# Kernel optimization log

Hardware: AMD Instinct MI355X
Metric: run time of the kernel (lower is better)

The kernel has to match this reference:

```python
import jax, jax.numpy as jnp
import numpy as np

N = 100000
E = 600000
NODE_DIM = 128
EDGE_DIM = 32
HIDDEN = 128  # must equal NODE_DIM (index_add_ into zeros_like(node_features))


def _linear_params(key, fan_in, fan_out):
    kw, kb = jax.random.split(key)
    bound = 1.0 / np.sqrt(fan_in)
    W = jax.random.uniform(kw, (fan_in, fan_out), minval=-bound, maxval=bound, dtype=jnp.float32)
    b = jax.random.uniform(kb, (fan_out,), minval=-bound, maxval=bound, dtype=jnp.float32)
    return W, b


def setup_inputs() -> dict:
    key = jax.random.key(0)
    ks = jax.random.split(key, 8)
    node_features = jax.random.normal(ks[0], (N, NODE_DIM), dtype=jnp.float32)
    edge_index = jax.random.randint(ks[1], (2, E), 0, N, dtype=jnp.int32)
    edge_features = jax.random.normal(ks[2], (E, EDGE_DIM), dtype=jnp.float32)
    m_W1, m_b1 = _linear_params(ks[3], 2 * NODE_DIM + EDGE_DIM, HIDDEN)
    m_W2, m_b2 = _linear_params(ks[4], HIDDEN, HIDDEN)
    a_W, a_b = _linear_params(ks[5], HIDDEN, 1)
    u_W1, u_b1 = _linear_params(ks[6], NODE_DIM + HIDDEN, HIDDEN)
    u_W2, u_b2 = _linear_params(ks[7], HIDDEN, NODE_DIM)
    return {
        "node_features": node_features,
        "edge_features": edge_features,
        "m_W1": m_W1, "m_b1": m_b1, "m_W2": m_W2, "m_b2": m_b2,
        "a_W": a_W, "a_b": a_b,
        "u_W1": u_W1, "u_b1": u_b1, "u_W2": u_W2, "u_b2": u_b2,
        "edge_index": edge_index,
    }


def reference(node_features, edge_features, m_W1, m_b1, m_W2, m_b2,
              a_W, a_b, u_W1, u_b1, u_W2, u_b2, edge_index):
    row, col = edge_index[0], edge_index[1]
    # gather endpoints + edge feats -> [E, 2*node_dim + edge_dim]
    msg_in = jnp.concatenate([node_features[row], node_features[col], edge_features], axis=-1)
    # message MLP
    h = jax.nn.relu(msg_in @ m_W1 + m_b1)
    messages = h @ m_W2 + m_b2  # [E, hidden]
    # global softmax over all edges (dim=0), per attention column (width 1)
    attn = jax.nn.softmax(messages @ a_W + a_b, axis=0)  # [E, 1]
    messages = messages * attn
    # scatter-add into destination nodes
    aggregated = jax.ops.segment_sum(messages, col, num_segments=node_features.shape[0])
    # update MLP + residual
    upd_in = jnp.concatenate([node_features, aggregated], axis=-1)
    u = jax.nn.relu(upd_in @ u_W1 + u_b1)
    updated = u @ u_W2 + u_b2
    return updated + node_features
```

## Files before the change

### kernel.cpp

```cpp
#include <hip/hip_runtime.h>
#include <hip/hip_bf16.h>
#include <hip/hip_fp8.h>
#include <stdint.h>

#define NN 100000
#define NE 600000
#define ND 128
#define ED 32
#define HID 128
#define SCANB 391
#define NEB 4688

using short8 = __attribute__((ext_vector_type(8))) short;
using f32x4  = __attribute__((ext_vector_type(4))) float;
using f32x2  = __attribute__((ext_vector_type(2))) float;

__device__ __forceinline__ uint32_t f2bf(float f) {
  uint32_t u = __float_as_uint(f);
  return (u + 0x7FFFu + ((u >> 16) & 1u)) >> 16;
}
__device__ __forceinline__ float bf2f(uint32_t h) {
  return __uint_as_float(h << 16);
}
__device__ __forceinline__ short8 pack8(float4 a, float4 b) {
  short8 s;
  s[0] = (short)f2bf(a.x); s[1] = (short)f2bf(a.y);
  s[2] = (short)f2bf(a.z); s[3] = (short)f2bf(a.w);
  s[4] = (short)f2bf(b.x); s[5] = (short)f2bf(b.y);
  s[6] = (short)f2bf(b.z); s[7] = (short)f2bf(b.w);
  return s;
}

__device__ __forceinline__ uint8_t fp8_enc(float v) {
#if __has_builtin(__builtin_amdgcn_cvt_pk_fp8_f32)
  return (uint8_t)(__builtin_amdgcn_cvt_pk_fp8_f32(v, v, 0, false) & 0xFF);
#else
  __hip_fp8_e4m3 q(v);
  return q.__x;
#endif
}
__device__ __forceinline__ float2 fp8_dec2(uint32_t v) {
#if __has_builtin(__builtin_amdgcn_cvt_pk_f32_fp8)
  f32x2 r = __builtin_amdgcn_cvt_pk_f32_fp8((int)v, false);
  return make_float2(r[0], r[1]);
#else
  __hip_fp8_e4m3 qa, qb;
  qa.__x = (uint8_t)(v & 0xFF); qb.__x = (uint8_t)((v >> 8) & 0xFF);
  return make_float2((float)qa, (float)qb);
#endif
}

__global__ __launch_bounds__(256) void k_prep_all(
    const float* __restrict__ uW1, const float* __restrict__ uW2,
    const float* __restrict__ W1, const float* __restrict__ W2,
    short* __restrict__ U1p, short* __restrict__ U2p,
    uint8_t* __restrict__ W1p8, uint8_t* __restrict__ W2p8) {
  int o = blockIdx.x * 256 + threadIdx.x;
  const float* src; int rel; int isFp8;
  short* dstS = nullptr; uint8_t* dst8 = nullptr;
  if (o < 32768)       { rel = o;         src = uW1; dstS = U1p;  isFp8 = 0; }
  else if (o < 49152)  { rel = o - 32768; src = uW2; dstS = U2p;  isFp8 = 0; }
  else if (o < 86016)  { rel = o - 49152; src = W1;  dst8 = W1p8; isFp8 = 1; }
  else if (o < 102400) { rel = o - 86016; src = W2;  dst8 = W2p8; isFp8 = 1; }
  else return;
  int j = rel & 7, c16 = (rel >> 3) & 15, g = (rel >> 7) & 3, nt = (rel >> 9) & 7, c = rel >> 12;
  int k = c * 32 + g * 8 + j, n = nt * 16 + c16;
  float v = src[k * 128 + n];
  if (isFp8) dst8[rel] = fp8_enc(v);
  else       dstS[rel] = (short)f2bf(v);
}

__global__ __launch_bounds__(256) void k_prep_nf(const float* __restrict__ nf,
                                                 short* __restrict__ nfb,
                                                 uint8_t* __restrict__ nfb8,
                                                 int* __restrict__ cnt) {
  const int total = NN * ND / 8;
  int gid = blockIdx.x * 256 + threadIdx.x;
  for (int i = gid; i < NN; i += gridDim.x * 256) cnt[i] = 0;
  for (int u = gid; u < total; u += gridDim.x * 256) {
    const float* s = nf + (size_t)u * 8;
    float4 v0 = *(const float4*)s, v1 = *(const float4*)(s + 4);
    *(short8*)(nfb + (size_t)u * 8) = pack8(v0, v1);
    uint8_t b[8];
    b[0] = fp8_enc(v0.x); b[1] = fp8_enc(v0.y); b[2] = fp8_enc(v0.z); b[3] = fp8_enc(v0.w);
    b[4] = fp8_enc(v1.x); b[5] = fp8_enc(v1.y); b[6] = fp8_enc(v1.z); b[7] = fp8_enc(v1.w);
    *(uint2*)(nfb8 + (size_t)u * 8) = *(const uint2*)b;
  }
}

__global__ __launch_bounds__(256, 3) void k_edge_mfma(
    const uint8_t* __restrict__ nfb8, const float* __restrict__ ef,
    const uint8_t* __restrict__ W1p8, const float* __restrict__ b1,
    const uint8_t* __restrict__ W2p8, const float* __restrict__ b2,
    const float* __restrict__ aW, const int* __restrict__ ei,
    const int* __restrict__ perm,
    uint8_t* __restrict__ msg8, float* __restrict__ logits) {
  __shared__ __align__(16) uint8_t sRow[128 * 136];
  __shared__ __align__(16) uint8_t sCol[128 * 136];
  __shared__ __align__(16) uint8_t sEf[128 * 40];
  __shared__ __align__(16) uint8_t sB8[2][4096];
  __shared__ int sIdx[256];
  __shared__ int sPerm[128];

  const int tid = threadIdx.x;
  const int wv = tid >> 6, ln = tid & 63, cr = ln & 15, gp = ln >> 4;
  const int e0 = blockIdx.x * 128;
  const int wrow = wv * 32;

  if (tid < 128) {
    int e = e0 + tid; if (e >= NE) e = NE - 1;
    sIdx[tid] = ei[e];
    sIdx[128 + tid] = ei[NE + e];
    sPerm[tid] = perm[e];
  }
  __syncthreads();

#pragma unroll
  for (int it = 0; it < 16; ++it) {
    int t = it * 256 + tid;
    int side = t >> 11;
    int r = (t & 2047) >> 4;
    int o = (t & 15) * 8;
    const uint8_t* src = nfb8 + (size_t)sIdx[side * 128 + r] * ND + o;
    uint8_t* dst = (side ? sCol : sRow) + r * 136 + o;
    *(uint2*)dst = *(const uint2*)src;
  }
#pragma unroll
  for (int it = 0; it < 2; ++it) {
    int u = it * 256 + tid;
    int r = u >> 2, o = (u & 3) * 8;
    int e = e0 + r; if (e >= NE) e = NE - 1;
    const float* src = ef + (size_t)e * ED + o;
    float4 v0 = *(const float4*)src, v1 = *(const float4*)(src + 4);
    uint8_t b[8];
    b[0] = fp8_enc(v0.x); b[1] = fp8_enc(v0.y); b[2] = fp8_enc(v0.z); b[3] = fp8_enc(v0.w);
    b[4] = fp8_enc(v1.x); b[5] = fp8_enc(v1.y); b[6] = fp8_enc(v1.z); b[7] = fp8_enc(v1.w);
    *(uint2*)&sEf[r * 40 + o] = *(const uint2*)b;
  }
  *(uint4*)&sB8[0][tid * 16] = *(const uint4*)(W1p8 + tid * 16);

  float bia[8], aWr[8], bia2[8];
#pragma unroll
  for (int nt = 0; nt < 8; ++nt) {
    bia[nt] = b1[nt * 16 + cr];
    bia2[nt] = b2[nt * 16 + cr];
    aWr[nt] = aW[nt * 16 + cr];
  }
  f32x4 acc[2][8];
#pragma unroll
  for (int mt = 0; mt < 2; ++mt)
#pragma unroll
    for (int nt = 0; nt < 8; ++nt)
      acc[mt][nt] = (f32x4){bia[nt], bia[nt], bia[nt], bia[nt]};
  __syncthreads();

  for (int c = 0; c < 9; ++c) {
    if (c < 8)
      *(uint4*)&sB8[(c + 1) & 1][tid * 16] =
          *(const uint4*)(W1p8 + (c + 1) * 4096 + tid * 16);
    const uint8_t* aSrc = (c < 4) ? (sRow + c * 32)
                        : (c < 8) ? (sCol + (c - 4) * 32) : sEf;
    const int pitch = (c == 8) ? 40 : 136;
    long af0 = *(const long*)(aSrc + (wrow + cr) * pitch + gp * 8);
    long af1 = *(const long*)(aSrc + (wrow + 16 + cr) * pitch + gp * 8);
    const uint8_t* bbuf = sB8[c & 1];
#pragma unroll
    for (int nt = 0; nt < 8; ++nt) {
      long bfr = *(const long*)&bbuf[(nt * 4 + gp) * 128 + cr * 8];
      acc[0][nt] = __builtin_amdgcn_mfma_f32_16x16x32_fp8_fp8(af0, bfr, acc[0][nt], 0, 0, 0);
      acc[1][nt] = __builtin_amdgcn_mfma_f32_16x16x32_fp8_fp8(af1, bfr, acc[1][nt], 0, 0, 0);
    }
    __syncthreads();
  }

#pragma unroll
  for (int mt = 0; mt < 2; ++mt)
#pragma unroll
    for (int nt = 0; nt < 8; ++nt)
#pragma unroll
      for (int rr = 0; rr < 4; ++rr)
        sRow[(wrow + mt * 16 + gp * 4 + rr) * 136 + nt * 16 + cr] =
            fp8_enc(fmaxf(acc[mt][nt][rr], 0.f));
  *(uint4*)&sB8[0][tid * 16] = *(const uint4*)(W2p8 + tid * 16);
  __syncthreads();

  f32x4 acc2[2][8];
#pragma unroll
  for (int mt = 0; mt < 2; ++mt)
#pragma unroll
    for (int nt = 0; nt < 8; ++nt)
      acc2[mt][nt] = (f32x4){bia2[nt], bia2[nt], bia2[nt], bia2[nt]};
  for (int c2 = 0; c2 < 4; ++c2) {
    if (c2 < 3)
      *(uint4*)&sB8[(c2 + 1) & 1][tid * 16] =
          *(const uint4*)(W2p8 + (c2 + 1) * 4096 + tid * 16);
    long af0 = *(const long*)&sRow[(wrow + cr) * 136 + c2 * 32 + gp * 8];
    long af1 = *(const long*)&sRow[(wrow + 16 + cr) * 136 + c2 * 32 + gp * 8];
    const uint8_t* bbuf = sB8[c2 & 1];
#pragma unroll
    for (int nt = 0; nt < 8; ++nt) {
      long bfr = *(const long*)&bbuf[(nt * 4 + gp) * 128 + cr * 8];
      acc2[0][nt] = __builtin_amdgcn_mfma_f32_16x16x32_fp8_fp8(af0, bfr, acc2[0][nt], 0, 0, 0);
      acc2[1][nt] = __builtin_amdgcn_mfma_f32_16x16x32_fp8_fp8(af1, bfr, acc2[1][nt], 0, 0, 0);
    }
    __syncthreads();
  }

#pragma unroll
  for (int mt = 0; mt < 2; ++mt)
#pragma unroll
    for (int rr = 0; rr < 4; ++rr) {
      float p = 0.f;
#pragma unroll
      for (int nt = 0; nt < 8; ++nt) p += acc2[mt][nt][rr] * aWr[nt];
      p += __shfl_xor(p, 1, 64);
      p += __shfl_xor(p, 2, 64);
      p += __shfl_xor(p, 4, 64);
      p += __shfl_xor(p, 8, 64);
      int row = wrow + mt * 16 + gp * 4 + rr;
      if (cr == 0 && e0 + row < NE) logits[sPerm[row]] = p;
    }

#pragma unroll
  for (int mt = 0; mt < 2; ++mt)
#pragma unroll
    for (int nt = 0; nt < 8; ++nt)
#pragma unroll
      for (int rr = 0; rr < 4; ++rr)
        sCol[(wrow + mt * 16 + gp * 4 + rr) * 136 + nt * 16 + cr] =
            fp8_enc(acc2[mt][nt][rr]);
  __syncthreads();
#pragma unroll
  for (int it = 0; it < 8; ++it) {
    int row = it * 16 + (tid >> 4), o8 = (tid & 15) * 8;
    if (e0 + row < NE)
      *(uint2*)(msg8 + (size_t)sPerm[row] * HID + o8) = *(const uint2*)&sCol[row * 136 + o8];
  }
}

__global__ __launch_bounds__(256, 4) void k_node_mfma(
    const short* __restrict__ nfb, const short* __restrict__ aggb,
    const short* __restrict__ U1p, const float* __restrict__ b1,
    const short* __restrict__ U2p, const float* __restrict__ b2,
    float* __restrict__ out) {
  __shared__ __align__(16) short sH[128 * 136];

  const int tid = threadIdx.x;
  const int wv = tid >> 6, ln = tid & 63, cr = ln & 15, gp = ln >> 4;
  const int n0 = blockIdx.x * 128;
  const int wrow = wv * 32;

  int na0 = n0 + wrow + cr;      if (na0 >= NN) na0 = NN - 1;
  int na1 = n0 + wrow + 16 + cr; if (na1 >= NN) na1 = NN - 1;

  float bia[8], bia2[8];
#pragma unroll
  for (int nt = 0; nt < 8; ++nt) {
    bia[nt] = b1[nt * 16 + cr];
    bia2[nt] = b2[nt * 16 + cr];
  }
  f32x4 acc[2][8];
#pragma unroll
  for (int mt = 0; mt < 2; ++mt)
#pragma unroll
    for (int nt = 0; nt < 8; ++nt)
      acc[mt][nt] = (f32x4){bia[nt], bia[nt], bia[nt], bia[nt]};

#pragma unroll
  for (int c = 0; c < 8; ++c) {
    const short* base = (c < 4) ? nfb : aggb;
    const int ko = (c & 3) * 32 + gp * 8;
    short8 af0 = *(const short8*)(base + (size_t)na0 * ND + ko);
    short8 af1 = *(const short8*)(base + (size_t)na1 * ND + ko);
    const short* Wc = U1p + c * 4096;
#pragma unroll
    for (int nt = 0; nt < 8; ++nt) {
      short8 bfr = *(const short8*)(Wc + (nt * 4 + gp) * 128 + cr * 8);
      acc[0][nt] = __builtin_amdgcn_mfma_f32_16x16x32_bf16(af0, bfr, acc[0][nt], 0, 0, 0);
      acc[1][nt] = __builtin_amdgcn_mfma_f32_16x16x32_bf16(af1, bfr, acc[1][nt], 0, 0, 0);
    }
  }

#pragma unroll
  for (int mt = 0; mt < 2; ++mt)
#pragma unroll
    for (int nt = 0; nt < 8; ++nt)
#pragma unroll
      for (int rr = 0; rr < 4; ++rr)
        sH[(wrow + mt * 16 + gp * 4 + rr) * 136 + nt * 16 + cr] =
            (short)f2bf(fmaxf(acc[mt][nt][rr], 0.f));

  f32x4 acc2[2][8];
#pragma unroll
  for (int mt = 0; mt < 2; ++mt)
#pragma unroll
    for (int nt = 0; nt < 8; ++nt)
      acc2[mt][nt] = (f32x4){bia2[nt], bia2[nt], bia2[nt], bia2[nt]};
#pragma unroll
  for (int c2 = 0; c2 < 4; ++c2) {
    short8 af0 = *(const short8*)&sH[(wrow + cr) * 136 + c2 * 32 + gp * 8];
    short8 af1 = *(const short8*)&sH[(wrow + 16 + cr) * 136 + c2 * 32 + gp * 8];
    const short* Wc = U2p + c2 * 4096;
#pragma unroll
    for (int nt = 0; nt < 8; ++nt) {
      short8 bfr = *(const short8*)(Wc + (nt * 4 + gp) * 128 + cr * 8);
      acc2[0][nt] = __builtin_amdgcn_mfma_f32_16x16x32_bf16(af0, bfr, acc2[0][nt], 0, 0, 0);
      acc2[1][nt] = __builtin_amdgcn_mfma_f32_16x16x32_bf16(af1, bfr, acc2[1][nt], 0, 0, 0);
    }
  }

#pragma unroll
  for (int mt = 0; mt < 2; ++mt)
#pragma unroll
    for (int rr = 0; rr < 4; ++rr) {
      int n = n0 + wrow + mt * 16 + gp * 4 + rr;
      if (n < NN) {
#pragma unroll
        for (int nt = 0; nt < 8; ++nt) {
          int col = nt * 16 + cr;
          float r = bf2f((uint16_t)nfb[(size_t)n * ND + col]);
          out[(size_t)n * ND + col] = acc2[mt][nt][rr] + r;
        }
      }
    }
}

__device__ __forceinline__ void ms_combine(float& m, float& s, float m2, float s2) {
  float M = fmaxf(m, m2);
  s = s * expf(m - M) + s2 * expf(m2 - M);
  m = M;
}
__device__ __forceinline__ void ms_block_reduce(float& m, float& s) {
#pragma unroll
  for (int o = 1; o < 64; o <<= 1) {
    float m2 = __shfl_xor(m, o, 64), s2 = __shfl_xor(s, o, 64);
    ms_combine(m, s, m2, s2);
  }
  __shared__ float sm[4], ss[4];
  if ((threadIdx.x & 63) == 0) { sm[threadIdx.x >> 6] = m; ss[threadIdx.x >> 6] = s; }
  __syncthreads();
  m = sm[0]; s = ss[0];
  ms_combine(m, s, sm[1], ss[1]);
  ms_combine(m, s, sm[2], ss[2]);
  ms_combine(m, s, sm[3], ss[3]);
}
__global__ __launch_bounds__(256) void k_red_p(const float* __restrict__ logits,
                                               float* __restrict__ pmax,
                                               float* __restrict__ psum) {
  float m = -3.402823466e38f, s = 0.f;
  for (int i = blockIdx.x * 256 + threadIdx.x; i < NE; i += 1024 * 256) {
    float l = logits[i];
    if (l <= m) s += expf(l - m);
    else { s = s * expf(m - l) + 1.f; m = l; }
  }
  ms_block_reduce(m, s);
  if (threadIdx.x == 0) { pmax[blockIdx.x] = m; psum[blockIdx.x] = s; }
}
__global__ __launch_bounds__(256) void k_red_f(const float* __restrict__ pmax,
                                               const float* __restrict__ psum,
                                               float* __restrict__ red) {
  float m = pmax[threadIdx.x], s = psum[threadIdx.x];
  ms_combine(m, s, pmax[threadIdx.x + 256], psum[threadIdx.x + 256]);
  ms_combine(m, s, pmax[threadIdx.x + 512], psum[threadIdx.x + 512]);
  ms_combine(m, s, pmax[threadIdx.x + 768], psum[threadIdx.x + 768]);
  ms_block_reduce(m, s);
  if (threadIdx.x == 0) { red[0] = m; red[1] = 1.0f / s; }
}

__global__ __launch_bounds__(256) void k_hist(const int* __restrict__ ei,
                                              int* __restrict__ cnt) {
  int e = blockIdx.x * 256 + threadIdx.x;
  if (e < NE) atomicAdd(&cnt[ei[NE + e]], 1);
}
__global__ __launch_bounds__(256) void k_scan_bsum(const int* __restrict__ cnt,
                                                   int* __restrict__ bsum) {
  int i = blockIdx.x * 256 + threadIdx.x;
  int v = (i < NN) ? cnt[i] : 0;
#pragma unroll
  for (int s = 1; s < 64; s <<= 1) v += __shfl_xor(v, s, 64);
  __shared__ int sv[4];
  if ((threadIdx.x & 63) == 0) sv[threadIdx.x >> 6] = v;
  __syncthreads();
  if (threadIdx.x == 0) bsum[blockIdx.x] = sv[0] + sv[1] + sv[2] + sv[3];
}
__global__ __launch_bounds__(512) void k_scan_boff(const int* __restrict__ bsum,
                                                   int* __restrict__ boff,
                                                   int* __restrict__ rowptr) {
  __shared__ int s[512];
  int t = threadIdx.x;
  int v = (t < SCANB) ? bsum[t] : 0;
  s[t] = v;
  __syncthreads();
  for (int off = 1; off < 512; off <<= 1) {
    int u = (t >= off) ? s[t - off] : 0;
    __syncthreads();
    s[t] += u;
    __syncthreads();
  }
  if (t < SCANB) boff[t] = s[t] - v;
  if (t == 0) rowptr[NN] = NE;
}
__global__ __launch_bounds__(256) void k_scan_final(int* __restrict__ cnt,
                                                    const int* __restrict__ boff,
                                                    int* __restrict__ rowptr) {
  __shared__ int s[256];
  int b = blockIdx.x, t = threadIdx.x, i = b * 256 + t;
  int v = (i < NN) ? cnt[i] : 0;
  s[t] = v;
  __syncthreads();
  for (int off = 1; off < 256; off <<= 1) {
    int u = (t >= off) ? s[t - off] : 0;
    __syncthreads();
    s[t] += u;
    __syncthreads();
  }
  int excl = s[t] - v + boff[b];
  if (i < NN) { rowptr[i] = excl; cnt[i] = excl; }
}
__global__ __launch_bounds__(256) void k_fill(const int* __restrict__ ei,
                                              int* __restrict__ cursor,
                                              int* __restrict__ perm) {
  int e = blockIdx.x * 256 + threadIdx.x;
  if (e >= NE) return;
  int c = ei[NE + e];
  int pos = atomicAdd(&cursor[c], 1);
  perm[e] = pos;
}

__global__ __launch_bounds__(256) void k_agg(
    const uint8_t* __restrict__ msg8, const float* __restrict__ logits,
    const int* __restrict__ rowptr, const float* __restrict__ red,
    short* __restrict__ aggb) {
  int n = blockIdx.x * 4 + (threadIdx.x >> 6);
  int lane = threadIdx.x & 63;
  if (n >= NN) return;
  float gm = red[0], inv = red[1];
  int i0 = rowptr[n], i1 = rowptr[n + 1];
  float a0 = 0.f, a1 = 0.f;
  for (int i = i0; i < i1; ++i) {
    float wt = expf(logits[i] - gm) * inv;
    uint32_t pk = *(const uint16_t*)(msg8 + (size_t)i * HID + lane * 2);
    float2 d = fp8_dec2(pk);
    a0 += wt * d.x;
    a1 += wt * d.y;
  }
  uint32_t packed = f2bf(a0) | (f2bf(a1) << 16);
  *(uint32_t*)(aggb + (size_t)n * ND + lane * 2) = packed;
}

extern "C" void kernel_launch(void* const* d_in, const int* in_sizes, int n_in,
                              void* d_out, int out_size, void* d_ws, size_t ws_size,
                              hipStream_t stream) {
  const float* nf  = (const float*)d_in[0];
  const float* ef  = (const float*)d_in[1];
  const float* mW1 = (const float*)d_in[2];
  const float* mb1 = (const float*)d_in[3];
  const float* mW2 = (const float*)d_in[4];
  const float* mb2 = (const float*)d_in[5];
  const float* aW  = (const float*)d_in[6];
  const float* uW1 = (const float*)d_in[8];
  const float* ub1 = (const float*)d_in[9];
  const float* uW2 = (const float*)d_in[10];
  const float* ub2 = (const float*)d_in[11];
  const int*   ei  = (const int*)d_in[12];
  float* out = (float*)d_out;

  char* ws = (char*)d_ws;
  uint8_t* msg8 = (uint8_t*)ws;
  float* logits = (float*)(ws + 76800000);
  float* pmax = (float*)(ws + 79200000);
  float* psum = pmax + 1024;
  float* red  = psum + 1024;
  uint8_t* W1p8 = (uint8_t*)(ws + 79208256);
  uint8_t* W2p8 = W1p8 + 36864;
  short* U1p = (short*)(W2p8 + 16384);
  short* U2p = U1p + 32768;
  int* rowptr = (int*)(ws + 79413056);
  int* cnt    = rowptr + (NN + 1);
  int* perm   = cnt + NN;
  int* bsum   = perm + NE;
  int* boff   = bsum + 512;
  short* nfb  = (short*)(ws + 82620000);
  uint8_t* nfb8 = (uint8_t*)(ws + 108220000);
  short* aggb = (short*)(ws + 121020000);

  k_prep_all<<<400, 256, 0, stream>>>(uW1, uW2, mW1, mW2, U1p, U2p, W1p8, W2p8);
  k_prep_nf<<<2048, 256, 0, stream>>>(nf, nfb, nfb8, cnt);
  k_hist<<<(NE + 255) / 256, 256, 0, stream>>>(ei, cnt);
  k_scan_bsum<<<SCANB, 256, 0, stream>>>(cnt, bsum);
  k_scan_boff<<<1, 512, 0, stream>>>(bsum, boff, rowptr);
  k_scan_final<<<SCANB, 256, 0, stream>>>(cnt, boff, rowptr);
  k_fill<<<(NE + 255) / 256, 256, 0, stream>>>(ei, cnt, perm);
  k_edge_mfma<<<NEB, 256, 0, stream>>>(nfb8, ef, W1p8, mb1, W2p8, mb2, aW, ei, perm,
                                       msg8, logits);
  k_red_p<<<1024, 256, 0, stream>>>(logits, pmax, psum);
  k_red_f<<<1, 256, 0, stream>>>(pmax, psum, red);
  k_agg<<<(NN + 3) / 4, 256, 0, stream>>>(msg8, logits, rowptr, red, aggb);
  k_node_mfma<<<(NN + 127) / 128, 256, 0, stream>>>(nfb, aggb, U1p, ub1, U2p, ub2, out);
}
```

Baseline: 295.9 us.

## Shrink edge-kernel LDS: single-buffer weights, load edge features into registers

Edge features are now loaded and converted to fp8 directly into the per-lane MFMA A-operand registers instead of being staged through shared memory. The weight chunk buffer drops from double to single buffering. Launch bounds rise from 3 to 4 blocks per CU. Together these cut LDS use so more blocks can be resident, at the cost of two barriers per chunk and no overlap between the weight loads and the MFMAs.

```diff
diff --git a/kernel.cpp b/kernel.cpp
--- a/kernel.cpp
+++ b/kernel.cpp
@@ -48,6 +48,14 @@
   qa.__x = (uint8_t)(v & 0xFF); qb.__x = (uint8_t)((v >> 8) & 0xFF);
   return make_float2((float)qa, (float)qb);
 #endif
+}
+__device__ __forceinline__ long pack_fp8x8(float4 a, float4 b) {
+  union { uint8_t u8[8]; long l; } u;
+  u.u8[0] = fp8_enc(a.x); u.u8[1] = fp8_enc(a.y);
+  u.u8[2] = fp8_enc(a.z); u.u8[3] = fp8_enc(a.w);
+  u.u8[4] = fp8_enc(b.x); u.u8[5] = fp8_enc(b.y);
+  u.u8[6] = fp8_enc(b.z); u.u8[7] = fp8_enc(b.w);
+  return u.l;
 }
 
 __global__ __launch_bounds__(256) void k_prep_all(
@@ -88,7 +96,7 @@
   }
 }
 
-__global__ __launch_bounds__(256, 3) void k_edge_mfma(
+__global__ __launch_bounds__(256, 4) void k_edge_mfma(
     const uint8_t* __restrict__ nfb8, const float* __restrict__ ef,
     const uint8_t* __restrict__ W1p8, const float* __restrict__ b1,
     const uint8_t* __restrict__ W2p8, const float* __restrict__ b2,
@@ -97,8 +105,7 @@
     uint8_t* __restrict__ msg8, float* __restrict__ logits) {
   __shared__ __align__(16) uint8_t sRow[128 * 136];
   __shared__ __align__(16) uint8_t sCol[128 * 136];
-  __shared__ __align__(16) uint8_t sEf[128 * 40];
-  __shared__ __align__(16) uint8_t sB8[2][4096];
+  __shared__ __align__(16) uint8_t sB8[4096];
   __shared__ int sIdx[256];
   __shared__ int sPerm[128];
 
@@ -125,19 +132,16 @@
     uint8_t* dst = (side ? sCol : sRow) + r * 136 + o;
     *(uint2*)dst = *(const uint2*)src;
   }
-#pragma unroll
-  for (int it = 0; it < 2; ++it) {
-    int u = it * 256 + tid;
-    int r = u >> 2, o = (u & 3) * 8;
-    int e = e0 + r; if (e >= NE) e = NE - 1;
-    const float* src = ef + (size_t)e * ED + o;
-    float4 v0 = *(const float4*)src, v1 = *(const float4*)(src + 4);
-    uint8_t b[8];
-    b[0] = fp8_enc(v0.x); b[1] = fp8_enc(v0.y); b[2] = fp8_enc(v0.z); b[3] = fp8_enc(v0.w);
-    b[4] = fp8_enc(v1.x); b[5] = fp8_enc(v1.y); b[6] = fp8_enc(v1.z); b[7] = fp8_enc(v1.w);
-    *(uint2*)&sEf[r * 40 + o] = *(const uint2*)b;
-  }
-  *(uint4*)&sB8[0][tid * 16] = *(const uint4*)(W1p8 + tid * 16);
+
+  long efA0, efA1;
+  {
+    int ea = e0 + wrow + cr;      if (ea >= NE) ea = NE - 1;
+    int eb = e0 + wrow + 16 + cr; if (eb >= NE) eb = NE - 1;
+    const float* f0 = ef + (size_t)ea * ED + gp * 8;
+    const float* f1 = ef + (size_t)eb * ED + gp * 8;
+    efA0 = pack_fp8x8(*(const float4*)f0, *(const float4*)(f0 + 4));
+    efA1 = pack_fp8x8(*(const float4*)f1, *(const float4*)(f1 + 4));
+  }
 
   float bia[8], aWr[8], bia2[8];
 #pragma unroll
@@ -152,25 +156,25 @@
 #pragma unroll
     for (int nt = 0; nt < 8; ++nt)
       acc[mt][nt] = (f32x4){bia[nt], bia[nt], bia[nt], bia[nt]};
-  __syncthreads();
 
   for (int c = 0; c < 9; ++c) {
-    if (c < 8)
-      *(uint4*)&sB8[(c + 1) & 1][tid * 16] =
-          *(const uint4*)(W1p8 + (c + 1) * 4096 + tid * 16);
-    const uint8_t* aSrc = (c < 4) ? (sRow + c * 32)
-                        : (c < 8) ? (sCol + (c - 4) * 32) : sEf;
-    const int pitch = (c == 8) ? 40 : 136;
-    long af0 = *(const long*)(aSrc + (wrow + cr) * pitch + gp * 8);
-    long af1 = *(const long*)(aSrc + (wrow + 16 + cr) * pitch + gp * 8);
-    const uint8_t* bbuf = sB8[c & 1];
+    __syncthreads();
+    *(uint4*)&sB8[tid * 16] = *(const uint4*)(W1p8 + c * 4096 + tid * 16);
+    __syncthreads();
+    long af0, af1;
+    if (c < 8) {
+      const uint8_t* aSrc = (c < 4) ? (sRow + c * 32) : (sCol + (c - 4) * 32);
+      af0 = *(const long*)(aSrc + (wrow + cr) * 136 + gp * 8);
+      af1 = *(const long*)(aSrc + (wrow + 16 + cr) * 136 + gp * 8);
+    } else {
+      af0 = efA0; af1 = efA1;
+    }
 #pragma unroll
     for (int nt = 0; nt < 8; ++nt) {
-      long bfr = *(const long*)&bbuf[(nt * 4 + gp) * 128 + cr * 8];
+      long bfr = *(const long*)&sB8[(nt * 4 + gp) * 128 + cr * 8];
       acc[0][nt] = __builtin_amdgcn_mfma_f32_16x16x32_fp8_fp8(af0, bfr, acc[0][nt], 0, 0, 0);
       acc[1][nt] = __builtin_amdgcn_mfma_f32_16x16x32_fp8_fp8(af1, bfr, acc[1][nt], 0, 0, 0);
     }
-    __syncthreads();
   }
 
 #pragma unroll
@@ -181,8 +185,6 @@
       for (int rr = 0; rr < 4; ++rr)
         sRow[(wrow + mt * 16 + gp * 4 + rr) * 136 + nt * 16 + cr] =
             fp8_enc(fmaxf(acc[mt][nt][rr], 0.f));
-  *(uint4*)&sB8[0][tid * 16] = *(const uint4*)(W2p8 + tid * 16);
-  __syncthreads();
 
   f32x4 acc2[2][8];
 #pragma unroll
@@ -191,19 +193,17 @@
     for (int nt = 0; nt < 8; ++nt)
       acc2[mt][nt] = (f32x4){bia2[nt], bia2[nt], bia2[nt], bia2[nt]};
   for (int c2 = 0; c2 < 4; ++c2) {
-    if (c2 < 3)
-      *(uint4*)&sB8[(c2 + 1) & 1][tid * 16] =
-          *(const uint4*)(W2p8 + (c2 + 1) * 4096 + tid * 16);
+    __syncthreads();
+    *(uint4*)&sB8[tid * 16] = *(const uint4*)(W2p8 + c2 * 4096 + tid * 16);
+    __syncthreads();
     long af0 = *(const long*)&sRow[(wrow + cr) * 136 + c2 * 32 + gp * 8];
     long af1 = *(const long*)&sRow[(wrow + 16 + cr) * 136 + c2 * 32 + gp * 8];
-    const uint8_t* bbuf = sB8[c2 & 1];
 #pragma unroll
     for (int nt = 0; nt < 8; ++nt) {
-      long bfr = *(const long*)&bbuf[(nt * 4 + gp) * 128 + cr * 8];
+      long bfr = *(const long*)&sB8[(nt * 4 + gp) * 128 + cr * 8];
       acc2[0][nt] = __builtin_amdgcn_mfma_f32_16x16x32_fp8_fp8(af0, bfr, acc2[0][nt], 0, 0, 0);
       acc2[1][nt] = __builtin_amdgcn_mfma_f32_16x16x32_fp8_fp8(af1, bfr, acc2[1][nt], 0, 0, 0);
     }
-    __syncthreads();
   }
 
 #pragma unroll
```

After: 294.8 us (median of 2 runs). About the same (-0.4%).
